# Performance work log

Hardware: AMD Instinct MI355X
Metric: run time of the kernel (lower is better)

The kernel has to match this reference:

```python
import jax, jax.numpy as jnp
import numpy as np

S, D_MODEL, D_RNN = 256, 512, 512  # module's broadcasting requires d_rnn == d_model


def setup_inputs() -> dict:
    key = jax.random.key(0)
    k1, k2, k3, k4 = jax.random.split(key, 4)
    x = jax.random.normal(k1, (S, D_MODEL), dtype=jnp.float32)
    state = jnp.zeros((D_RNN, D_MODEL), dtype=jnp.float32)
    # equinox nn.Linear default init: U[-1/sqrt(in), 1/sqrt(in)] for weight and bias
    lim = 1.0 / np.sqrt(D_MODEL)
    W1 = jax.random.uniform(k2, (2 * D_RNN, D_MODEL), minval=-lim, maxval=lim, dtype=jnp.float32)
    b1 = jax.random.uniform(k3, (2 * D_RNN,), minval=-lim, maxval=lim, dtype=jnp.float32)
    # Lambda init exactly as in source: inv_sigmoid(p) = log(1/(1-p)), bounds ** (1/8)
    inv_sig = lambda p: np.log(1.0 / (1.0 - p))
    lower = float(np.power(inv_sig(0.9), 1.0 / 8.0))
    upper = float(np.power(inv_sig(0.999), 1.0 / 8.0))
    Lambda = jax.random.uniform(k4, (D_MODEL,), minval=lower, maxval=upper, dtype=jnp.float32)
    return {"x": x, "state": state, "W1": W1, "b1": b1, "Lambda": Lambda}


def reference(x, state, W1, b1, Lambda):
    # lin1 applied per timestep: (S, d_model) @ (d_model, 2*d_rnn)
    z = jax.nn.sigmoid(x @ W1.T + b1)              # (S, 2*d_rnn)
    inp, rec = jnp.split(z, 2, axis=-1)            # each (S, d_rnn)
    # recurrence gate a_t in (0,1): exp(-8 * softplus(Lambda) * rec)
    a = jnp.exp(-8.0 * jax.nn.softplus(Lambda)[None, :] * rec)  # (S, d_rnn)
    # gated input: outer product per step -> (S, d_rnn, d_model)
    gated_x = jnp.einsum('is,is,id->isd', jnp.sqrt(1.0 - a * a), inp, x)

    def step(h, xs):
        g, at = xs
        h = at[:, None] * h + g                    # (d_rnn, d_model)
        return h, h

    state, y = jax.lax.scan(step, state, (gated_x, a))
    return (y, state)
```

## Files before the change

### kernel.cpp

```cpp
#include <hip/hip_runtime.h>
#include <hip/hip_bf16.h>

#define S_LEN 256
#define DM    512
#define DR    512

typedef float f4 __attribute__((ext_vector_type(4)));
typedef float f2 __attribute__((ext_vector_type(2)));


__global__ __launch_bounds__(256) void k_transpose_x(const float* __restrict__ x,
                                                     float* __restrict__ xT) {
    __shared__ float tile[32][33];
    const int k0 = blockIdx.x * 32;
    const int t0 = blockIdx.y * 32;
    const int lx = threadIdx.x & 31;
    const int ly = threadIdx.x >> 5;
#pragma unroll
    for (int i = 0; i < 32; i += 8)
        tile[ly + i][lx] = x[(t0 + ly + i) * DM + k0 + lx];
    __syncthreads();
#pragma unroll
    for (int i = 0; i < 32; i += 8)
        xT[(k0 + ly + i) * S_LEN + t0 + lx] = tile[lx][ly + i];
}

__global__ __launch_bounds__(256) void k_gemm(const float* __restrict__ xT,
                                              const float* __restrict__ W1,
                                              float* __restrict__ part) {
    const int bx = blockIdx.x;
    const int sp = bx >> 2;
    const int kq = bx & 3;
    const int t  = threadIdx.x;

    const int r0 = 2 * sp, r1 = 2 * sp + 1;
    const int r2 = DR + 2 * sp, r3 = DR + 2 * sp + 1;

    const f4* __restrict__ W0 = reinterpret_cast<const f4*>(W1 + r0 * DM + kq * 128);
    const f4* __restrict__ W1p = reinterpret_cast<const f4*>(W1 + r1 * DM + kq * 128);
    const f4* __restrict__ W2 = reinterpret_cast<const f4*>(W1 + r2 * DM + kq * 128);
    const f4* __restrict__ W3 = reinterpret_cast<const f4*>(W1 + r3 * DM + kq * 128);
    const float* __restrict__ xb = xT + (kq * 128) * S_LEN + t;

    float a0 = 0.f, a1 = 0.f, a2 = 0.f, a3 = 0.f;

#pragma unroll 4
    for (int kk = 0; kk < 32; ++kk) {
        const float x0 = xb[(4 * kk + 0) * S_LEN];
        const float x1 = xb[(4 * kk + 1) * S_LEN];
        const float x2 = xb[(4 * kk + 2) * S_LEN];
        const float x3 = xb[(4 * kk + 3) * S_LEN];
        const f4 w0 = W0[kk];
        const f4 w1 = W1p[kk];
        const f4 w2 = W2[kk];
        const f4 w3 = W3[kk];
        a0 = fmaf(x0, w0.x, a0); a0 = fmaf(x1, w0.y, a0);
        a0 = fmaf(x2, w0.z, a0); a0 = fmaf(x3, w0.w, a0);
        a1 = fmaf(x0, w1.x, a1); a1 = fmaf(x1, w1.y, a1);
        a1 = fmaf(x2, w1.z, a1); a1 = fmaf(x3, w1.w, a1);
        a2 = fmaf(x0, w2.x, a2); a2 = fmaf(x1, w2.y, a2);
        a2 = fmaf(x2, w2.z, a2); a2 = fmaf(x3, w2.w, a2);
        a3 = fmaf(x0, w3.x, a3); a3 = fmaf(x1, w3.y, a3);
        a3 = fmaf(x2, w3.z, a3); a3 = fmaf(x3, w3.w, a3);
    }

    float* __restrict__ pb = part + kq * (1024 * 256);
    pb[r0 * 256 + t] = a0;
    pb[r1 * 256 + t] = a1;
    pb[r2 * 256 + t] = a2;
    pb[r3 * 256 + t] = a3;
}

__global__ __launch_bounds__(256) void k_act2(const float* __restrict__ part,
                                              const float* __restrict__ b1,
                                              const float* __restrict__ Lam,
                                              f2* __restrict__ acT) {
    const int s = blockIdx.x;
    const int t = threadIdx.x;
    const int P = 1024 * 256;

    const float pre_i = part[s * 256 + t]            + part[P + s * 256 + t]
                      + part[2 * P + s * 256 + t]    + part[3 * P + s * 256 + t]
                      + b1[s];
    const float pre_r = part[(DR + s) * 256 + t]         + part[P + (DR + s) * 256 + t]
                      + part[2 * P + (DR + s) * 256 + t] + part[3 * P + (DR + s) * 256 + t]
                      + b1[DR + s];

    const float inp = 1.f / (1.f + expf(-pre_i));
    const float rec = 1.f / (1.f + expf(-pre_r));
    const float sof = log1pf(expf(Lam[s]));
    const float a   = expf(-8.f * sof * rec);
    const float c   = sqrtf(fmaxf(1.f - a * a, 0.f)) * inp;
    f2 ac; ac.x = a; ac.y = c;
    acT[s * S_LEN + t] = ac;
}

__global__ __launch_bounds__(256) void k_rec(const float* __restrict__ x,
                                             const float* __restrict__ state0,
                                             const f2* __restrict__ acT,
                                             f4* __restrict__ out4) {
    const int bx   = blockIdx.x;
    const int sp   = (bx & 7) * 32 + (bx >> 3);
    const int tid  = threadIdx.x;
    const int half = tid >> 7;
    const int s    = sp * 2 + half;
    const int dq   = tid & 127;

    __shared__ f2 ac_l[2][S_LEN];
    f2* lf = &ac_l[0][0];
    lf[tid]       = acT[sp * 2 * S_LEN + tid];
    lf[tid + 256] = acT[sp * 2 * S_LEN + tid + 256];
    __syncthreads();

    const f4* __restrict__ st4 = reinterpret_cast<const f4*>(state0);
    f4 h = st4[s * 128 + dq];

    const f4* __restrict__ x4 = reinterpret_cast<const f4*>(x);
    f4 xv = x4[dq];

#pragma unroll 4
    for (int t = 0; t < S_LEN; ++t) {
        f4 xn;
        if (t + 1 < S_LEN) xn = x4[(t + 1) * 128 + dq];
        else xn = (f4)0.f;

        const f2 ac = ac_l[half][t];
        const float at = ac.x, ct = ac.y;
        h.x = fmaf(at, h.x, ct * xv.x);
        h.y = fmaf(at, h.y, ct * xv.y);
        h.z = fmaf(at, h.z, ct * xv.z);
        h.w = fmaf(at, h.w, ct * xv.w);

        __builtin_nontemporal_store(h, &out4[(t * DR + s) * 128 + dq]);
        xv = xn;
    }
    out4[(S_LEN * DR) * 128 + s * 128 + dq] = h;
}

extern "C" void kernel_launch(void* const* d_in, const int* in_sizes, int n_in,
                              void* d_out, int out_size, void* d_ws, size_t ws_size,
                              hipStream_t stream) {
    const float* x      = (const float*)d_in[0];
    const float* state0 = (const float*)d_in[1];
    const float* W1     = (const float*)d_in[2];
    const float* b1     = (const float*)d_in[3];
    const float* Lam    = (const float*)d_in[4];

    float* ws   = (float*)d_ws;
    float* xT   = ws;
    float* part = ws + 131072;
    f2*    acT  = (f2*)(ws + 1179648);

    f4* out4 = (f4*)d_out;

    k_transpose_x<<<dim3(16, 8), 256, 0, stream>>>(x, xT);
    k_gemm<<<dim3(1024), 256, 0, stream>>>(xT, W1, part);
    k_act2<<<dim3(512), 256, 0, stream>>>(part, b1, Lam, acT);
    k_rec<<<dim3(256), 256, 0, stream>>>(x, state0, acT, out4);
}
```

Before: 64.79 us.

## Split GEMM reduction eight ways and fuse activation into recurrence kernel

The projection GEMM now splits the 512-long reduction into eight 64-wide slices, running 2048 blocks instead of 1024. The separate activation kernel is removed. Each recurrence block now sums the eight partial results itself, adds the bias, and computes the gate and coefficient into shared memory before its scan. This saves one kernel launch and the round trip of the gate array through global memory. In exchange the partial-sum buffer doubles in size, the workspace needs to be larger, and every recurrence block does extra global reads before its sequential loop can start.

```diff
diff --git a/kernel.cpp b/kernel.cpp
--- a/kernel.cpp
+++ b/kernel.cpp
@@ -29,29 +29,29 @@
                                               const float* __restrict__ W1,
                                               float* __restrict__ part) {
     const int bx = blockIdx.x;
-    const int sp = bx >> 2;
-    const int kq = bx & 3;
+    const int sp = bx >> 3;
+    const int ke = bx & 7;
     const int t  = threadIdx.x;
 
     const int r0 = 2 * sp, r1 = 2 * sp + 1;
     const int r2 = DR + 2 * sp, r3 = DR + 2 * sp + 1;
 
-    const f4* __restrict__ W0 = reinterpret_cast<const f4*>(W1 + r0 * DM + kq * 128);
-    const f4* __restrict__ W1p = reinterpret_cast<const f4*>(W1 + r1 * DM + kq * 128);
-    const f4* __restrict__ W2 = reinterpret_cast<const f4*>(W1 + r2 * DM + kq * 128);
-    const f4* __restrict__ W3 = reinterpret_cast<const f4*>(W1 + r3 * DM + kq * 128);
-    const float* __restrict__ xb = xT + (kq * 128) * S_LEN + t;
+    const f4* __restrict__ W0 = reinterpret_cast<const f4*>(W1 + r0 * DM + ke * 64);
+    const f4* __restrict__ Wp = reinterpret_cast<const f4*>(W1 + r1 * DM + ke * 64);
+    const f4* __restrict__ W2 = reinterpret_cast<const f4*>(W1 + r2 * DM + ke * 64);
+    const f4* __restrict__ W3 = reinterpret_cast<const f4*>(W1 + r3 * DM + ke * 64);
+    const float* __restrict__ xb = xT + (ke * 64) * S_LEN + t;
 
     float a0 = 0.f, a1 = 0.f, a2 = 0.f, a3 = 0.f;
 
 #pragma unroll 4
-    for (int kk = 0; kk < 32; ++kk) {
+    for (int kk = 0; kk < 16; ++kk) {
         const float x0 = xb[(4 * kk + 0) * S_LEN];
         const float x1 = xb[(4 * kk + 1) * S_LEN];
         const float x2 = xb[(4 * kk + 2) * S_LEN];
         const float x3 = xb[(4 * kk + 3) * S_LEN];
         const f4 w0 = W0[kk];
-        const f4 w1 = W1p[kk];
+        const f4 w1 = Wp[kk];
         const f4 w2 = W2[kk];
         const f4 w3 = W3[kk];
         a0 = fmaf(x0, w0.x, a0); a0 = fmaf(x1, w0.y, a0);
@@ -64,40 +64,18 @@
         a3 = fmaf(x2, w3.z, a3); a3 = fmaf(x3, w3.w, a3);
     }
 
-    float* __restrict__ pb = part + kq * (1024 * 256);
+    float* __restrict__ pb = part + ke * (1024 * 256);
     pb[r0 * 256 + t] = a0;
     pb[r1 * 256 + t] = a1;
     pb[r2 * 256 + t] = a2;
     pb[r3 * 256 + t] = a3;
 }
 
-__global__ __launch_bounds__(256) void k_act2(const float* __restrict__ part,
-                                              const float* __restrict__ b1,
-                                              const float* __restrict__ Lam,
-                                              f2* __restrict__ acT) {
-    const int s = blockIdx.x;
-    const int t = threadIdx.x;
-    const int P = 1024 * 256;
-
-    const float pre_i = part[s * 256 + t]            + part[P + s * 256 + t]
-                      + part[2 * P + s * 256 + t]    + part[3 * P + s * 256 + t]
-                      + b1[s];
-    const float pre_r = part[(DR + s) * 256 + t]         + part[P + (DR + s) * 256 + t]
-                      + part[2 * P + (DR + s) * 256 + t] + part[3 * P + (DR + s) * 256 + t]
-                      + b1[DR + s];
-
-    const float inp = 1.f / (1.f + expf(-pre_i));
-    const float rec = 1.f / (1.f + expf(-pre_r));
-    const float sof = log1pf(expf(Lam[s]));
-    const float a   = expf(-8.f * sof * rec);
-    const float c   = sqrtf(fmaxf(1.f - a * a, 0.f)) * inp;
-    f2 ac; ac.x = a; ac.y = c;
-    acT[s * S_LEN + t] = ac;
-}
-
 __global__ __launch_bounds__(256) void k_rec(const float* __restrict__ x,
                                              const float* __restrict__ state0,
-                                             const f2* __restrict__ acT,
+                                             const float* __restrict__ part,
+                                             const float* __restrict__ b1,
+                                             const float* __restrict__ Lam,
                                              f4* __restrict__ out4) {
     const int bx   = blockIdx.x;
     const int sp   = (bx & 7) * 32 + (bx >> 3);
@@ -107,16 +85,37 @@
     const int dq   = tid & 127;
 
     __shared__ f2 ac_l[2][S_LEN];
-    f2* lf = &ac_l[0][0];
-    lf[tid]       = acT[sp * 2 * S_LEN + tid];
-    lf[tid + 256] = acT[sp * 2 * S_LEN + tid + 256];
-    __syncthreads();
+
+    const int P = 1024 * 256;
+#pragma unroll
+    for (int sl = 0; sl < 2; ++sl) {
+        const int srow = sp * 2 + sl;
+        const int tt   = tid;
+        if (tt < S_LEN) {
+            float pi = b1[srow];
+            float pr = b1[DR + srow];
+#pragma unroll
+            for (int e = 0; e < 8; ++e) {
+                pi += part[e * P + srow * 256 + tt];
+                pr += part[e * P + (DR + srow) * 256 + tt];
+            }
+            const float inp = 1.f / (1.f + expf(-pi));
+            const float rec = 1.f / (1.f + expf(-pr));
+            const float sof = log1pf(expf(Lam[srow]));
+            const float a   = expf(-8.f * sof * rec);
+            const float c   = sqrtf(fmaxf(1.f - a * a, 0.f)) * inp;
+            f2 ac; ac.x = a; ac.y = c;
+            ac_l[sl][tt] = ac;
+        }
+    }
 
     const f4* __restrict__ st4 = reinterpret_cast<const f4*>(state0);
     f4 h = st4[s * 128 + dq];
 
     const f4* __restrict__ x4 = reinterpret_cast<const f4*>(x);
     f4 xv = x4[dq];
+
+    __syncthreads();
 
 #pragma unroll 4
     for (int t = 0; t < S_LEN; ++t) {
@@ -149,12 +148,10 @@
     float* ws   = (float*)d_ws;
     float* xT   = ws;
     float* part = ws + 131072;
-    f2*    acT  = (f2*)(ws + 1179648);
 
     f4* out4 = (f4*)d_out;
 
     k_transpose_x<<<dim3(16, 8), 256, 0, stream>>>(x, xT);
-    k_gemm<<<dim3(1024), 256, 0, stream>>>(xT, W1, part);
-    k_act2<<<dim3(512), 256, 0, stream>>>(part, b1, Lam, acT);
-    k_rec<<<dim3(256), 256, 0, stream>>>(x, state0, acT, out4);
+    k_gemm<<<dim3(2048), 256, 0, stream>>>(xT, W1, part);
+    k_rec<<<dim3(256), 256, 0, stream>>>(x, state0, part, b1, Lam, out4);
 }
```

New measurement: 63.82 us. About the same (-1.5%).
